# Kernel optimization log

Hardware: AMD Instinct MI355X
Metric: run time of the kernel (lower is better)

## Reference

```python
import math
import jax, jax.numpy as jnp
import numpy as np

B, Q, K = 1, 2048, 2048
CQ = CK = CV = 128
H, CH = 8, 32
HD = H * CH  # 256


def setup_inputs() -> dict:
    key = jax.random.key(0)
    ks = jax.random.split(key, 12)
    s = 0.02
    return {
        "q_x": jax.random.normal(ks[0], (B, Q, CQ), jnp.float32),
        "kv_x": jax.random.normal(ks[1], (B, K, CK), jnp.float32),
        "bias": jax.random.normal(ks[2], (B, 1, Q, K), jnp.float32),
        "distance": jax.random.uniform(ks[3], (B, Q, K, H), jnp.float32),
        "Wq": jax.random.normal(ks[4], (CQ, HD), jnp.float32) * s,
        "Wk": jax.random.normal(ks[5], (CK, HD), jnp.float32) * s,
        "Wv": jax.random.normal(ks[6], (CV, HD), jnp.float32) * s,
        "Wg": jax.random.normal(ks[7], (CQ, HD), jnp.float32) * s,
        "bg": jnp.zeros((HD,), jnp.float32),
        "Wo": jax.random.normal(ks[8], (HD, CQ), jnp.float32) * s,
        "bo": jnp.zeros((CQ,), jnp.float32),
    }


def reference(q_x, kv_x, bias, distance, Wq, Wk, Wv, Wg, bg, Wo, bo):
    # Projections -> [B, S, H, CH]
    q = (q_x @ Wq).reshape(B, Q, H, CH) / math.sqrt(CH)
    k = (kv_x @ Wk).reshape(B, K, H, CH)
    v = (kv_x @ Wv).reshape(B, K, H, CH)
    # Scores [B, H, Q, K]
    a = jnp.einsum("bqhc,bkhc->bhqk", q, k)
    a = a + bias
    # mha_permu=True: distance [B,Q,K,H] -> [B,H,Q,K]; rel_dis_pair_bias='add'
    a = a + jnp.transpose(distance, (0, 3, 1, 2))
    a = jax.nn.softmax(a, axis=-1)
    o = jnp.einsum("bhqk,bkhc->bqhc", a, v)  # [B, Q, H, CH]
    # Gating
    g = jax.nn.sigmoid(q_x @ Wg + bg).reshape(B, Q, H, CH)
    o = o * g
    o = o.reshape(B, Q, HD)
    return o @ Wo + bo
```

## Files before the change

kernel.cpp:

```cpp
#include <hip/hip_runtime.h>
#include <hip/hip_bf16.h>

#define Qn 2048
#define Kn 2048
#define Cin 128
#define Hn 8
#define CHn 32
#define HDn 256
#define NSPLIT 8

typedef __attribute__((ext_vector_type(8))) short short8;
typedef __attribute__((ext_vector_type(4))) float f32x4;

static __device__ __forceinline__ unsigned short f2bf(float f) {
    unsigned int u = __float_as_uint(f);
    u += 0x7fffu + ((u >> 16) & 1u);
    return (unsigned short)(u >> 16);
}

__global__ __launch_bounds__(256) void proj_kernel(
    const float* __restrict__ qx, const float* __restrict__ kvx,
    const float* __restrict__ Wq, const float* __restrict__ Wk,
    const float* __restrict__ Wv, const float* __restrict__ Wg,
    const float* __restrict__ bg,
    unsigned short* __restrict__ qb, unsigned short* __restrict__ kb,
    unsigned short* __restrict__ vtb, float* __restrict__ gb)
{
    const int mat = blockIdx.y;
    const int r0 = blockIdx.x * 8;
    const int j = threadIdx.x;
    const float* A = (mat == 0 || mat == 3) ? qx : kvx;
    const float* W = (mat == 0) ? Wq : (mat == 1) ? Wk : (mat == 2) ? Wv : Wg;
    const float* Ar = A + r0 * Cin;
    float acc[8] = {0.f, 0.f, 0.f, 0.f, 0.f, 0.f, 0.f, 0.f};
    for (int c = 0; c < Cin; ++c) {
        const float w = W[c * HDn + j];
        #pragma unroll
        for (int i = 0; i < 8; ++i)
            acc[i] = fmaf(Ar[i * Cin + c], w, acc[i]);
    }
    if (mat == 0) {
        const float s = 0.17677669529663687f;
        #pragma unroll
        for (int i = 0; i < 8; ++i)
            qb[(r0 + i) * HDn + j] = f2bf(acc[i] * s);
    } else if (mat == 1) {
        #pragma unroll
        for (int i = 0; i < 8; ++i)
            kb[(r0 + i) * HDn + j] = f2bf(acc[i]);
    } else if (mat == 2) {
        unsigned short tmp[8];
        #pragma unroll
        for (int i = 0; i < 8; ++i) tmp[i] = f2bf(acc[i]);
        *(short8*)(vtb + (size_t)j * Kn + r0) = *(short8*)tmp;
    } else {
        const float b = bg[j];
        #pragma unroll
        for (int i = 0; i < 8; ++i)
            gb[(r0 + i) * HDn + j] = 1.f / (1.f + __expf(-(acc[i] + b)));
    }
}

__global__ __launch_bounds__(512, 4) void attn_kernel(
    const unsigned short* __restrict__ qb, const unsigned short* __restrict__ kb,
    const unsigned short* __restrict__ vtb,
    const float* __restrict__ bias, const float* __restrict__ dist,
    float* __restrict__ opart, float* __restrict__ lpart)
{
    __shared__ unsigned short ps[Hn][16][72];

    const int bx = blockIdx.x;
    const int qt = bx >> 3;
    const int sp = bx & 7;
    const int q0 = qt * 16;
    const int k00 = sp * 256;
    const int t = threadIdx.x;
    const int h = t >> 6;
    const int l = t & 63;
    const int g = l >> 4;
    const int n = l & 15;

    const short8 qf = *(const short8*)(qb + (q0 + n) * HDn + h * CHn + g * 8);

    f32x4 o0 = {0.f, 0.f, 0.f, 0.f};
    f32x4 o1 = {0.f, 0.f, 0.f, 0.f};
    float lacc[4] = {0.f, 0.f, 0.f, 0.f};
    unsigned short* psh = &ps[h][0][0];
    const f32x4 z = {0.f, 0.f, 0.f, 0.f};

    const float* dbase = dist + ((size_t)(q0 + g * 4) * Kn + k00 + n) * Hn + h;
    const float* bbase = bias + (size_t)(q0 + g * 4) * Kn + k00 + n;

    #pragma unroll
    for (int kt = 0; kt < 4; ++kt) {
        const int k0 = k00 + kt * 64;

        short8 kf[4];
        #pragma unroll
        for (int kkg = 0; kkg < 4; ++kkg)
            kf[kkg] = *(const short8*)(kb + (k0 + kkg * 16 + n) * HDn + h * CHn + g * 8);
        short8 vf[4];
        #pragma unroll
        for (int chunk = 0; chunk < 2; ++chunk) {
            vf[chunk * 2]     = *(const short8*)(vtb + (h * CHn + n) * Kn + k0 + chunk * 32 + g * 8);
            vf[chunk * 2 + 1] = *(const short8*)(vtb + (h * CHn + 16 + n) * Kn + k0 + chunk * 32 + g * 8);
        }
        __builtin_amdgcn_sched_barrier(0);

        float db[16], bb[16];
        #pragma unroll
        for (int r = 0; r < 4; ++r) {
            #pragma unroll
            for (int kk = 0; kk < 4; ++kk) {
                db[r * 4 + kk] = dbase[((size_t)r * Kn + kt * 64 + kk * 16) * Hn];
                bb[r * 4 + kk] = bbase[(size_t)r * Kn + kt * 64 + kk * 16];
            }
        }

        f32x4 sf[4];
        #pragma unroll
        for (int kkg = 0; kkg < 4; ++kkg)
            sf[kkg] = __builtin_amdgcn_mfma_f32_16x16x32_bf16(qf, kf[kkg], z, 0, 0, 0);

        #pragma unroll
        for (int kkg = 0; kkg < 4; ++kkg) {
            #pragma unroll
            for (int r = 0; r < 4; ++r) {
                const float p = __expf(sf[kkg][r] + db[r * 4 + kkg] + bb[r * 4 + kkg]);
                sf[kkg][r] = p;
                lacc[r] += p;
            }
        }

        #pragma unroll
        for (int kkg = 0; kkg < 4; ++kkg) {
            #pragma unroll
            for (int r = 0; r < 4; ++r)
                psh[(g * 4 + r) * 72 + kkg * 16 + n] = f2bf(sf[kkg][r]);
        }

        #pragma unroll
        for (int chunk = 0; chunk < 2; ++chunk) {
            const short8 pf = *(const short8*)(psh + n * 72 + chunk * 32 + g * 8);
            o0 = __builtin_amdgcn_mfma_f32_16x16x32_bf16(pf, vf[chunk * 2], o0, 0, 0, 0);
            o1 = __builtin_amdgcn_mfma_f32_16x16x32_bf16(pf, vf[chunk * 2 + 1], o1, 0, 0, 0);
        }
    }

    float* op = opart + (size_t)sp * (Qn * HDn);
    #pragma unroll
    for (int r = 0; r < 4; ++r) {
        const int qg = q0 + g * 4 + r;
        op[qg * HDn + h * CHn + n] = o0[r];
        op[qg * HDn + h * CHn + 16 + n] = o1[r];
        float v = lacc[r];
        v += __shfl_xor(v, 1);
        v += __shfl_xor(v, 2);
        v += __shfl_xor(v, 4);
        v += __shfl_xor(v, 8);
        lacc[r] = v;
    }
    if (n == 0) {
        float* lp = lpart + (size_t)sp * (Qn * Hn);
        #pragma unroll
        for (int r = 0; r < 4; ++r)
            lp[(q0 + g * 4 + r) * Hn + h] = lacc[r];
    }
}

__global__ __launch_bounds__(256) void mergeout_kernel(
    const float* __restrict__ opart, const float* __restrict__ lpart,
    const float* __restrict__ gb, const float* __restrict__ Wo,
    const float* __restrict__ bo, float* __restrict__ out)
{
    __shared__ float olds[HDn];
    __shared__ float red[4][128];
    const int q = blockIdx.x;
    const int t = threadIdx.x;
    const int h = t >> 5;
    float s = 0.f;
    #pragma unroll
    for (int sp = 0; sp < NSPLIT; ++sp)
        s += opart[(size_t)sp * (Qn * HDn) + q * HDn + t];
    float lt = 0.f;
    #pragma unroll
    for (int sp = 0; sp < NSPLIT; ++sp)
        lt += lpart[(size_t)sp * (Qn * Hn) + q * Hn + h];
    olds[t] = (s / lt) * gb[q * HDn + t];
    __syncthreads();
    const int p = t & 63;
    const int seg = t >> 6;
    float a0 = 0.f, a1 = 0.f;
    for (int c = seg * 64; c < seg * 64 + 64; ++c) {
        const float ov = olds[c];
        const float2 w = *(const float2*)(Wo + c * Cin + 2 * p);
        a0 = fmaf(ov, w.x, a0);
        a1 = fmaf(ov, w.y, a1);
    }
    red[seg][2 * p] = a0;
    red[seg][2 * p + 1] = a1;
    __syncthreads();
    if (t < 128)
        out[q * Cin + t] = red[0][t] + red[1][t] + red[2][t] + red[3][t] + bo[t];
}

extern "C" void kernel_launch(void* const* d_in, const int* in_sizes, int n_in,
                              void* d_out, int out_size, void* d_ws, size_t ws_size,
                              hipStream_t stream)
{
    const float* qx   = (const float*)d_in[0];
    const float* kvx  = (const float*)d_in[1];
    const float* bias = (const float*)d_in[2];
    const float* dist = (const float*)d_in[3];
    const float* Wq   = (const float*)d_in[4];
    const float* Wk   = (const float*)d_in[5];
    const float* Wv   = (const float*)d_in[6];
    const float* Wg   = (const float*)d_in[7];
    const float* bg   = (const float*)d_in[8];
    const float* Wo   = (const float*)d_in[9];
    const float* bo   = (const float*)d_in[10];
    float* out = (float*)d_out;

    char* w = (char*)d_ws;
    unsigned short* qb  = (unsigned short*)(w);
    unsigned short* kb  = (unsigned short*)(w + (1ull << 20));
    unsigned short* vtb = (unsigned short*)(w + (2ull << 20));
    float* gb    = (float*)(w + (3ull << 20));
    float* opart = (float*)(w + (5ull << 20));
    float* lpart = (float*)(w + (21ull << 20));

    proj_kernel<<<dim3(Qn / 8, 4), 256, 0, stream>>>(qx, kvx, Wq, Wk, Wv, Wg, bg, qb, kb, vtb, gb);
    attn_kernel<<<dim3(128 * NSPLIT), 512, 0, stream>>>(qb, kb, vtb, bias, dist, opart, lpart);
    mergeout_kernel<<<dim3(Qn), 256, 0, stream>>>(opart, lpart, gb, Wo, bo, out);
}
```

Before: 318.6 us.

## Stage distance and bias tiles into LDS with double-buffered async loads

The attention kernel now copies each 32-key tile of the distance and bias tensors into shared memory with the direct global-to-LDS load instruction. These copies are contiguous and coalesced, whereas before each head strided through the [Q,K,H] distance layout with scattered scalar loads. K/V fragments and the staged tiles are double-buffered so the next tile loads while the current one is computed, synchronized by a waitcnt plus barrier per tile. The cost is more shared memory per block, smaller key tiles, and a block-wide barrier every iteration.

```diff
diff --git a/kernel.cpp b/kernel.cpp
--- a/kernel.cpp
+++ b/kernel.cpp
@@ -16,6 +16,12 @@
     unsigned int u = __float_as_uint(f);
     u += 0x7fffu + ((u >> 16) & 1u);
     return (unsigned short)(u >> 16);
+}
+
+static __device__ __forceinline__ void ld16(const void* g, void* l) {
+    __builtin_amdgcn_global_load_lds(
+        (const __attribute__((address_space(1))) void*)g,
+        (__attribute__((address_space(3))) void*)l, 16, 0, 0);
 }
 
 __global__ __launch_bounds__(256) void proj_kernel(
@@ -67,7 +73,9 @@
     const float* __restrict__ bias, const float* __restrict__ dist,
     float* __restrict__ opart, float* __restrict__ lpart)
 {
-    __shared__ unsigned short ps[Hn][16][72];
+    __shared__ float dlds[2][16][32][8];
+    __shared__ float blds[2][16][32];
+    __shared__ unsigned short ps[Hn][16][40];
 
     const int bx = blockIdx.x;
     const int qt = bx >> 3;
@@ -88,64 +96,62 @@
     unsigned short* psh = &ps[h][0][0];
     const f32x4 z = {0.f, 0.f, 0.f, 0.f};
 
-    const float* dbase = dist + ((size_t)(q0 + g * 4) * Kn + k00 + n) * Hn + h;
-    const float* bbase = bias + (size_t)(q0 + g * 4) * Kn + k00 + n;
-
-    #pragma unroll
-    for (int kt = 0; kt < 4; ++kt) {
-        const int k0 = k00 + kt * 64;
-
-        short8 kf[4];
-        #pragma unroll
-        for (int kkg = 0; kkg < 4; ++kkg)
-            kf[kkg] = *(const short8*)(kb + (k0 + kkg * 16 + n) * HDn + h * CHn + g * 8);
-        short8 vf[4];
-        #pragma unroll
-        for (int chunk = 0; chunk < 2; ++chunk) {
-            vf[chunk * 2]     = *(const short8*)(vtb + (h * CHn + n) * Kn + k0 + chunk * 32 + g * 8);
-            vf[chunk * 2 + 1] = *(const short8*)(vtb + (h * CHn + 16 + n) * Kn + k0 + chunk * 32 + g * 8);
+    const float* dsrcA = dist + (size_t)(q0 + h) * Kn * Hn + l * 4;
+    const float* dsrcB = dist + (size_t)(q0 + h + 8) * Kn * Hn + l * 4;
+    const float* bsrc  = bias + (size_t)(q0 + h * 8 + (l >> 3)) * Kn + (l & 7) * 4;
+
+    short8 kf[2][2], vf[2][2];
+
+    #define STAGE(buf, kt_) do {                                              \
+        const int k0s = k00 + (kt_) * 32;                                     \
+        ld16(dsrcA + (size_t)k0s * 8, &dlds[buf][h][0][0]);                   \
+        ld16(dsrcB + (size_t)k0s * 8, &dlds[buf][h + 8][0][0]);               \
+        if (h < 2) ld16(bsrc + k0s, &blds[buf][h * 8][0]);                    \
+    } while (0)
+
+    #define KVLOAD(set, kt_) do {                                             \
+        const int k0v = k00 + (kt_) * 32;                                     \
+        kf[set][0] = *(const short8*)(kb + (k0v + n) * HDn + h * CHn + g * 8);      \
+        kf[set][1] = *(const short8*)(kb + (k0v + 16 + n) * HDn + h * CHn + g * 8); \
+        vf[set][0] = *(const short8*)(vtb + (h * CHn + n) * Kn + k0v + g * 8);      \
+        vf[set][1] = *(const short8*)(vtb + (h * CHn + 16 + n) * Kn + k0v + g * 8); \
+    } while (0)
+
+    KVLOAD(0, 0);
+    __builtin_amdgcn_sched_barrier(0);
+    STAGE(0, 0);
+
+    #pragma unroll
+    for (int kt = 0; kt < 8; ++kt) {
+        const int cur = kt & 1;
+        asm volatile("s_waitcnt vmcnt(0)\n\ts_barrier" ::: "memory");
+        if (kt < 7) {
+            KVLOAD(cur ^ 1, kt + 1);
+            __builtin_amdgcn_sched_barrier(0);
+            STAGE(cur ^ 1, kt + 1);
+            __builtin_amdgcn_sched_barrier(0);
         }
-        __builtin_amdgcn_sched_barrier(0);
-
-        float db[16], bb[16];
-        #pragma unroll
-        for (int r = 0; r < 4; ++r) {
+        f32x4 sf[2];
+        sf[0] = __builtin_amdgcn_mfma_f32_16x16x32_bf16(qf, kf[cur][0], z, 0, 0, 0);
+        sf[1] = __builtin_amdgcn_mfma_f32_16x16x32_bf16(qf, kf[cur][1], z, 0, 0, 0);
+        #pragma unroll
+        for (int kk = 0; kk < 2; ++kk) {
             #pragma unroll
-            for (int kk = 0; kk < 4; ++kk) {
-                db[r * 4 + kk] = dbase[((size_t)r * Kn + kt * 64 + kk * 16) * Hn];
-                bb[r * 4 + kk] = bbase[(size_t)r * Kn + kt * 64 + kk * 16];
+            for (int r = 0; r < 4; ++r) {
+                const float p = __expf(sf[kk][r]
+                                       + dlds[cur][g * 4 + r][kk * 16 + n][h]
+                                       + blds[cur][g * 4 + r][kk * 16 + n]);
+                sf[kk][r] = p;
+                lacc[r] += p;
+                psh[(g * 4 + r) * 40 + kk * 16 + n] = f2bf(p);
             }
         }
-
-        f32x4 sf[4];
-        #pragma unroll
-        for (int kkg = 0; kkg < 4; ++kkg)
-            sf[kkg] = __builtin_amdgcn_mfma_f32_16x16x32_bf16(qf, kf[kkg], z, 0, 0, 0);
-
-        #pragma unroll
-        for (int kkg = 0; kkg < 4; ++kkg) {
-            #pragma unroll
-            for (int r = 0; r < 4; ++r) {
-                const float p = __expf(sf[kkg][r] + db[r * 4 + kkg] + bb[r * 4 + kkg]);
-                sf[kkg][r] = p;
-                lacc[r] += p;
-            }
-        }
-
-        #pragma unroll
-        for (int kkg = 0; kkg < 4; ++kkg) {
-            #pragma unroll
-            for (int r = 0; r < 4; ++r)
-                psh[(g * 4 + r) * 72 + kkg * 16 + n] = f2bf(sf[kkg][r]);
-        }
-
-        #pragma unroll
-        for (int chunk = 0; chunk < 2; ++chunk) {
-            const short8 pf = *(const short8*)(psh + n * 72 + chunk * 32 + g * 8);
-            o0 = __builtin_amdgcn_mfma_f32_16x16x32_bf16(pf, vf[chunk * 2], o0, 0, 0, 0);
-            o1 = __builtin_amdgcn_mfma_f32_16x16x32_bf16(pf, vf[chunk * 2 + 1], o1, 0, 0, 0);
-        }
-    }
+        const short8 pf = *(const short8*)(psh + n * 40 + g * 8);
+        o0 = __builtin_amdgcn_mfma_f32_16x16x32_bf16(pf, vf[cur][0], o0, 0, 0, 0);
+        o1 = __builtin_amdgcn_mfma_f32_16x16x32_bf16(pf, vf[cur][1], o1, 0, 0, 0);
+    }
+    #undef STAGE
+    #undef KVLOAD
 
     float* op = opart + (size_t)sp * (Qn * HDn);
     #pragma unroll
```

Result: faster. 279.1 us (-12.4%).

## Stage distance+bias via coalesced loads into fp16 LDS ring, halve KV splits

Applied to the files above, without the earlier changes.

Distance and bias tiles are now loaded cooperatively with coalesced 16-byte reads, pre-summed, converted to fp16, and written into a triple-buffered LDS ring two tiles ahead of use. This replaces the old per-thread strided scalar gathers of distance across heads. NSPLIT drops from 8 to 4, so each block iterates over 8 KV tiles and the merge reads fewer partials. The cost is extra LDS traffic, a barrier per tile, fp16 rounding of the additive bias, and half as many blocks.

```diff
diff --git a/kernel.cpp b/kernel.cpp
--- a/kernel.cpp
+++ b/kernel.cpp
@@ -7,7 +7,12 @@
 #define Hn 8
 #define CHn 32
 #define HDn 256
-#define NSPLIT 8
+#define NSPLIT 4
+#define KVB 64
+#define NT 8
+#define DRW 72
+#define DPL (16 * DRW)
+#define DBUFH (Hn * DPL)
 
 typedef __attribute__((ext_vector_type(8))) short short8;
 typedef __attribute__((ext_vector_type(4))) float f32x4;
@@ -67,85 +72,107 @@
     const float* __restrict__ bias, const float* __restrict__ dist,
     float* __restrict__ opart, float* __restrict__ lpart)
 {
-    __shared__ unsigned short ps[Hn][16][72];
+    __shared__ _Float16 dl[3 * DBUFH];
+    __shared__ unsigned short ps[Hn * 16 * DRW];
 
     const int bx = blockIdx.x;
-    const int qt = bx >> 3;
-    const int sp = bx & 7;
+    const int qt = bx >> 2;
+    const int sp = bx & 3;
     const int q0 = qt * 16;
-    const int k00 = sp * 256;
+    const int k00 = sp * 512;
     const int t = threadIdx.x;
     const int h = t >> 6;
     const int l = t & 63;
     const int g = l >> 4;
     const int n = l & 15;
+    const int le = l & 1;
+    const int kc = l >> 1;
 
     const short8 qf = *(const short8*)(qb + (q0 + n) * HDn + h * CHn + g * 8);
 
     f32x4 o0 = {0.f, 0.f, 0.f, 0.f};
     f32x4 o1 = {0.f, 0.f, 0.f, 0.f};
     float lacc[4] = {0.f, 0.f, 0.f, 0.f};
-    unsigned short* psh = &ps[h][0][0];
+    unsigned short* psh = &ps[h * 16 * DRW];
     const f32x4 z = {0.f, 0.f, 0.f, 0.f};
 
-    const float* dbase = dist + ((size_t)(q0 + g * 4) * Kn + k00 + n) * Hn + h;
-    const float* bbase = bias + (size_t)(q0 + g * 4) * Kn + k00 + n;
-
-    #pragma unroll
-    for (int kt = 0; kt < 4; ++kt) {
-        const int k0 = k00 + kt * 64;
-
-        short8 kf[4];
+    f32x4 sreg[2][4];
+    float breg[2][4];
+
+    #define STAGELOAD(set, kt_) do {                                          \
+        const size_t kb0 = (size_t)(k00 + (kt_) * KVB);                       \
+        _Pragma("unroll") for (int rc = 0; rc < 4; ++rc) {                    \
+            const int qloc = h + 8 * (rc >> 1);                               \
+            const int c_ = rc & 1;                                            \
+            sreg[set][rc] = *(const f32x4*)(dist +                            \
+                ((size_t)(q0 + qloc) * Kn + kb0 + c_ * 32) * Hn + l * 4);     \
+            breg[set][rc] = bias[(size_t)(q0 + qloc) * Kn + kb0 + c_ * 32 + kc]; \
+        }                                                                     \
+    } while (0)
+
+    #define CW(set, buf) do {                                                 \
+        _Float16* db_ = dl + (buf) * DBUFH;                                   \
+        _Pragma("unroll") for (int rc = 0; rc < 4; ++rc) {                    \
+            const int qloc = h + 8 * (rc >> 1);                               \
+            const int c_ = rc & 1;                                            \
+            _Pragma("unroll") for (int j = 0; j < 4; ++j)                     \
+                db_[(4 * le + j) * DPL + qloc * DRW + c_ * 32 + kc] =         \
+                    (_Float16)(sreg[set][rc][j] + breg[set][rc]);             \
+        }                                                                     \
+    } while (0)
+
+    STAGELOAD(0, 0);
+    __builtin_amdgcn_sched_barrier(0);
+    STAGELOAD(1, 1);
+    __builtin_amdgcn_sched_barrier(0);
+    CW(0, 0);
+    asm volatile("s_waitcnt lgkmcnt(0)\n\ts_barrier" ::: "memory");
+
+    #pragma unroll
+    for (int kt = 0; kt < NT; ++kt) {
+        const int k0 = k00 + kt * KVB;
+
+        short8 kf[4], vf[2][2];
         #pragma unroll
         for (int kkg = 0; kkg < 4; ++kkg)
             kf[kkg] = *(const short8*)(kb + (k0 + kkg * 16 + n) * HDn + h * CHn + g * 8);
-        short8 vf[4];
-        #pragma unroll
-        for (int chunk = 0; chunk < 2; ++chunk) {
-            vf[chunk * 2]     = *(const short8*)(vtb + (h * CHn + n) * Kn + k0 + chunk * 32 + g * 8);
-            vf[chunk * 2 + 1] = *(const short8*)(vtb + (h * CHn + 16 + n) * Kn + k0 + chunk * 32 + g * 8);
+        #pragma unroll
+        for (int c = 0; c < 2; ++c) {
+            vf[c][0] = *(const short8*)(vtb + (h * CHn + n) * Kn + k0 + c * 32 + g * 8);
+            vf[c][1] = *(const short8*)(vtb + (h * CHn + 16 + n) * Kn + k0 + c * 32 + g * 8);
         }
         __builtin_amdgcn_sched_barrier(0);
-
-        float db[16], bb[16];
-        #pragma unroll
-        for (int r = 0; r < 4; ++r) {
-            #pragma unroll
-            for (int kk = 0; kk < 4; ++kk) {
-                db[r * 4 + kk] = dbase[((size_t)r * Kn + kt * 64 + kk * 16) * Hn];
-                bb[r * 4 + kk] = bbase[(size_t)r * Kn + kt * 64 + kk * 16];
-            }
-        }
+        if (kt + 2 < NT) { STAGELOAD(kt & 1, kt + 2); __builtin_amdgcn_sched_barrier(0); }
+        if (kt + 1 < NT) { CW((kt + 1) & 1, (kt + 1) % 3); }
+        if (kt + 1 < NT) { asm volatile("s_waitcnt lgkmcnt(0)\n\ts_barrier" ::: "memory"); }
 
         f32x4 sf[4];
         #pragma unroll
         for (int kkg = 0; kkg < 4; ++kkg)
             sf[kkg] = __builtin_amdgcn_mfma_f32_16x16x32_bf16(qf, kf[kkg], z, 0, 0, 0);
 
+        const _Float16* dc = dl + (kt % 3) * DBUFH + h * DPL;
         #pragma unroll
         for (int kkg = 0; kkg < 4; ++kkg) {
             #pragma unroll
             for (int r = 0; r < 4; ++r) {
-                const float p = __expf(sf[kkg][r] + db[r * 4 + kkg] + bb[r * 4 + kkg]);
+                const int q_l = g * 4 + r;
+                const float p = __expf(sf[kkg][r] + (float)dc[q_l * DRW + kkg * 16 + n]);
                 sf[kkg][r] = p;
                 lacc[r] += p;
+                psh[q_l * DRW + kkg * 16 + n] = f2bf(p);
             }
         }
 
         #pragma unroll
-        for (int kkg = 0; kkg < 4; ++kkg) {
-            #pragma unroll
-            for (int r = 0; r < 4; ++r)
-                psh[(g * 4 + r) * 72 + kkg * 16 + n] = f2bf(sf[kkg][r]);
+        for (int c = 0; c < 2; ++c) {
+            const short8 pf = *(const short8*)(psh + n * DRW + c * 32 + g * 8);
+            o0 = __builtin_amdgcn_mfma_f32_16x16x32_bf16(pf, vf[c][0], o0, 0, 0, 0);
+            o1 = __builtin_amdgcn_mfma_f32_16x16x32_bf16(pf, vf[c][1], o1, 0, 0, 0);
         }
-
-        #pragma unroll
-        for (int chunk = 0; chunk < 2; ++chunk) {
-            const short8 pf = *(const short8*)(psh + n * 72 + chunk * 32 + g * 8);
-            o0 = __builtin_amdgcn_mfma_f32_16x16x32_bf16(pf, vf[chunk * 2], o0, 0, 0, 0);
-            o1 = __builtin_amdgcn_mfma_f32_16x16x32_bf16(pf, vf[chunk * 2 + 1], o1, 0, 0, 0);
-        }
-    }
+    }
+    #undef STAGELOAD
+    #undef CW
 
     float* op = opart + (size_t)sp * (Qn * HDn);
     #pragma unroll
```

New measurement: 272.8 us. 1.17x faster.

## Pre-combine bias and distance into fp16 MFMA-layout buffer via prep kernel

Applied to the files above, without the earlier changes.

Adds a prep kernel that reads distance and bias with coalesced vector loads, adds them, converts the sum to fp16 and writes it, transposed through LDS, in the exact per-lane fragment order the attention kernel consumes. The attention kernel then loads two 16-byte vectors per tile instead of 32 strided scalar fp32 loads, and the P stores are fused into the exp loop. The cost is an extra pass over the full 128MB distance tensor plus a 64MB fp16 intermediate write and read, and fp16 rounding of the combined bias.

```diff
diff --git a/kernel.cpp b/kernel.cpp
--- a/kernel.cpp
+++ b/kernel.cpp
@@ -11,11 +11,53 @@
 
 typedef __attribute__((ext_vector_type(8))) short short8;
 typedef __attribute__((ext_vector_type(4))) float f32x4;
+typedef __attribute__((ext_vector_type(8))) _Float16 f16x8;
 
 static __device__ __forceinline__ unsigned short f2bf(float f) {
     unsigned int u = __float_as_uint(f);
     u += 0x7fffu + ((u >> 16) & 1u);
     return (unsigned short)(u >> 16);
+}
+
+__global__ __launch_bounds__(256) void prep_kernel(
+    const float* __restrict__ bias, const float* __restrict__ dist,
+    _Float16* __restrict__ pdb)
+{
+    __shared__ _Float16 lds[10240];
+    const int b = blockIdx.x;
+    const int kc = b & 7;
+    const int G = (b >> 3) & 3;
+    const int qt = b >> 5;
+    const int t = threadIdx.x;
+    const int q0 = qt * 16 + G * 4;
+    const int k0 = kc * 256;
+
+    #pragma unroll
+    for (int i = 0; i < 8; ++i) {
+        const int idx = i * 1024 + t * 4;
+        const int qr = idx >> 11;
+        const int k_l = (idx >> 3) & 255;
+        const int h0 = idx & 7;
+        const f32x4 v = *(const f32x4*)(dist + ((size_t)(q0 + qr) * Kn + k0 + k_l) * 8 + h0);
+        const float bb = bias[(size_t)(q0 + qr) * Kn + k0 + k_l];
+        const int n = k_l & 15;
+        const int kkg = (k_l >> 4) & 3;
+        const int ktl = k_l >> 6;
+        #pragma unroll
+        for (int j = 0; j < 4; ++j) {
+            const int f = ((h0 + j) * 4 + ktl) * 256 + n * 16 + kkg * 4 + qr;
+            lds[f + (f >> 5) * 8] = (_Float16)(v[j] + bb);
+        }
+    }
+    __syncthreads();
+    const int h = t >> 5;
+    const int ktl = (t >> 3) & 3;
+    const int nn = (t & 7) * 2;
+    _Float16* dst = pdb + (((size_t)(qt * 32 + kc * 4 + ktl) * 8 + h) << 10) + G * 256 + nn * 16;
+    const _Float16* src = lds + t * 40;
+    #pragma unroll
+    for (int i = 0; i < 4; ++i)
+        *(short8*)(dst + i * 8) = *(const short8*)(src + i * 8);
 }
 
 __global__ __launch_bounds__(256) void proj_kernel(
@@ -63,8 +105,7 @@
 
 __global__ __launch_bounds__(512, 4) void attn_kernel(
     const unsigned short* __restrict__ qb, const unsigned short* __restrict__ kb,
-    const unsigned short* __restrict__ vtb,
-    const float* __restrict__ bias, const float* __restrict__ dist,
+    const unsigned short* __restrict__ vtb, const _Float16* __restrict__ pdb,
     float* __restrict__ opart, float* __restrict__ lpart)
 {
     __shared__ unsigned short ps[Hn][16][72];
@@ -88,8 +129,7 @@
     unsigned short* psh = &ps[h][0][0];
     const f32x4 z = {0.f, 0.f, 0.f, 0.f};
 
-    const float* dbase = dist + ((size_t)(q0 + g * 4) * Kn + k00 + n) * Hn + h;
-    const float* bbase = bias + (size_t)(q0 + g * 4) * Kn + k00 + n;
+    const _Float16* pbase = pdb + ((((size_t)qt * 32 + sp * 4) * 8 + h) << 10) + (l << 4);
 
     #pragma unroll
     for (int kt = 0; kt < 4; ++kt) {
@@ -99,23 +139,14 @@
         #pragma unroll
         for (int kkg = 0; kkg < 4; ++kkg)
             kf[kkg] = *(const short8*)(kb + (k0 + kkg * 16 + n) * HDn + h * CHn + g * 8);
-        short8 vf[4];
-        #pragma unroll
-        for (int chunk = 0; chunk < 2; ++chunk) {
-            vf[chunk * 2]     = *(const short8*)(vtb + (h * CHn + n) * Kn + k0 + chunk * 32 + g * 8);
-            vf[chunk * 2 + 1] = *(const short8*)(vtb + (h * CHn + 16 + n) * Kn + k0 + chunk * 32 + g * 8);
-        }
-        __builtin_amdgcn_sched_barrier(0);
-
-        float db[16], bb[16];
-        #pragma unroll
-        for (int r = 0; r < 4; ++r) {
-            #pragma unroll
-            for (int kk = 0; kk < 4; ++kk) {
-                db[r * 4 + kk] = dbase[((size_t)r * Kn + kt * 64 + kk * 16) * Hn];
-                bb[r * 4 + kk] = bbase[(size_t)r * Kn + kt * 64 + kk * 16];
-            }
-        }
+        short8 vf[2][2];
+        #pragma unroll
+        for (int c = 0; c < 2; ++c) {
+            vf[c][0] = *(const short8*)(vtb + (h * CHn + n) * Kn + k0 + c * 32 + g * 8);
+            vf[c][1] = *(const short8*)(vtb + (h * CHn + 16 + n) * Kn + k0 + c * 32 + g * 8);
+        }
+        const f16x8 pa = *(const f16x8*)(pbase + (kt << 13));
+        const f16x8 pb = *(const f16x8*)(pbase + (kt << 13) + 8);
 
         f32x4 sf[4];
         #pragma unroll
@@ -126,24 +157,20 @@
         for (int kkg = 0; kkg < 4; ++kkg) {
             #pragma unroll
             for (int r = 0; r < 4; ++r) {
-                const float p = __expf(sf[kkg][r] + db[r * 4 + kkg] + bb[r * 4 + kkg]);
+                const int j = kkg * 4 + r;
+                const float dv = (float)((j < 8) ? pa[j & 7] : pb[j & 7]);
+                const float p = __expf(sf[kkg][r] + dv);
                 sf[kkg][r] = p;
                 lacc[r] += p;
+                psh[(g * 4 + r) * 72 + kkg * 16 + n] = f2bf(p);
             }
         }
 
         #pragma unroll
-        for (int kkg = 0; kkg < 4; ++kkg) {
-            #pragma unroll
-            for (int r = 0; r < 4; ++r)
-                psh[(g * 4 + r) * 72 + kkg * 16 + n] = f2bf(sf[kkg][r]);
-        }
-
-        #pragma unroll
-        for (int chunk = 0; chunk < 2; ++chunk) {
-            const short8 pf = *(const short8*)(psh + n * 72 + chunk * 32 + g * 8);
-            o0 = __builtin_amdgcn_mfma_f32_16x16x32_bf16(pf, vf[chunk * 2], o0, 0, 0, 0);
-            o1 = __builtin_amdgcn_mfma_f32_16x16x32_bf16(pf, vf[chunk * 2 + 1], o1, 0, 0, 0);
+        for (int c = 0; c < 2; ++c) {
+            const short8 pf = *(const short8*)(psh + n * 72 + c * 32 + g * 8);
+            o0 = __builtin_amdgcn_mfma_f32_16x16x32_bf16(pf, vf[c][0], o0, 0, 0, 0);
+            o1 = __builtin_amdgcn_mfma_f32_16x16x32_bf16(pf, vf[c][1], o1, 0, 0, 0);
         }
     }
 
@@ -228,8 +255,10 @@
     float* gb    = (float*)(w + (3ull << 20));
     float* opart = (float*)(w + (5ull << 20));
     float* lpart = (float*)(w + (21ull << 20));
-
+    _Float16* pdb = (_Float16*)(w + (24ull << 20));
+
+    prep_kernel<<<dim3(4096), 256, 0, stream>>>(bias, dist, pdb);
     proj_kernel<<<dim3(Qn / 8, 4), 256, 0, stream>>>(qx, kvx, Wq, Wk, Wv, Wg, bg, qb, kb, vtb, gb);
-    attn_kernel<<<dim3(128 * NSPLIT), 512, 0, stream>>>(qb, kb, vtb, bias, dist, opart, lpart);
+    attn_kernel<<<dim3(128 * NSPLIT), 512, 0, stream>>>(qb, kb, vtb, pdb, opart, lpart);
     mergeout_kernel<<<dim3(Qn), 256, 0, stream>>>(opart, lpart, gb, Wo, bo, out);
 }
```

Result: faster. 311.2 us (-2.3%).
